# Kernel tuning notes

Hardware: AMD Instinct MI355X
Metric: run time of the kernel (lower is better)

The kernel has to match this reference:

```python
import jax, jax.numpy as jnp
import numpy as np

IMG = 128
FX, FY, CX, CY = 588.03, 587.07, 320.0, 240.0
FLIP = 1.0
SAMPLE = 1024  # sample_num in Img2pcl
N_VERTS = 778


def setup_inputs() -> dict:
    key = jax.random.key(0)
    ks = jax.random.split(key, 6)
    B = 64
    real = jax.random.uniform(ks[0], (B, 1, IMG, IMG), jnp.float32)   # normalized depth in [0,1)
    synth = jax.random.uniform(ks[1], (B, 1, IMG, IMG), jnp.float32)  # unused by forward
    verts = jax.random.normal(ks[2], (B, N_VERTS, 3), jnp.float32)
    faces = jax.random.randint(ks[3], (1538, 3), 0, N_VERTS, jnp.int32)  # unused by forward
    center = jax.random.normal(ks[4], (B, 3), jnp.float32) * 0.1 + jnp.array([0.0, 0.0, 400.0], jnp.float32)
    # crop matrix must be invertible: identity plus small perturbation
    M = jnp.eye(3, dtype=jnp.float32)[None] + 0.1 * jax.random.normal(ks[5], (B, 3, 3), jnp.float32)
    cube = jnp.full((B, 3), 250.0, jnp.float32)
    return dict(real=real, synth=synth, verts=verts, faces=faces, center=center, M=M, cube=cube)


def _img2pcl(real, center, M, cube):
    """Vectorized Img2pcl: normalized (u,v,d) -> normalized xyz for every pixel, plus valid mask."""
    B = real.shape[0]
    # input already IMG x IMG so F.interpolate is identity
    img = real[:, 0]                                   # [B,H,W]
    t = 2.0 * jnp.arange(IMG, dtype=jnp.float32) / (IMG - 1.0) - 1.0
    mesh_x = jnp.broadcast_to(t[:, None], (IMG, IMG))  # varies along rows (v)
    mesh_y = jnp.broadcast_to(t[None, :], (IMG, IMG))  # varies along cols (u)
    uvd = jnp.stack([
        jnp.broadcast_to(mesh_y, (B, IMG, IMG)),
        jnp.broadcast_to(mesh_x, (B, IMG, IMG)),
        img,
    ], axis=-1).reshape(B, IMG * IMG, 3)               # [B,P,3]
    # unnormalize uv and depth
    uv = (uvd[..., :2] + 1.0) * (IMG / 2.0)
    d = uvd[..., 2] * (cube[:, None, 2] / 2.0) + center[:, None, 2]   # [B,P]
    # get_trans_points with M^{-1}
    M_inv = jnp.linalg.inv(M)                          # [B,3,3]
    h = jnp.concatenate([uv, jnp.ones_like(uv[..., :1])], axis=-1)    # [B,P,3]
    uv_w = jnp.einsum('bij,bpj->bpi', M_inv, h)[..., :2]
    # pointsImgTo3D (pinhole back-projection)
    x = (uv_w[..., 0] - CX) * d / FX
    y = FLIP * (uv_w[..., 1] - CY) * d / FY
    xyz = jnp.stack([x, y, d], axis=-1)                # [B,P,3]
    xyz_n = (xyz - center[:, None, :]) / (cube[:, None, :] / 2.0)
    mask = img.reshape(B, -1) <= 0.99                  # valid (foreground) pixels
    return xyz_n, mask


def reference(real, synth, verts, faces, center, M, cube):
    xyz, mask = _img2pcl(real, center, M, cube)
    # torch.multinomial(uniform weights, SAMPLE, without replacement) over valid pixels
    # == Gumbel top-k over the masked candidate set (jit-compatible, fixed shapes)
    u = jax.random.uniform(jax.random.key(1), mask.shape)
    gumbel = -jnp.log(-jnp.log(u + 1e-20) + 1e-20)
    score = jnp.where(mask, gumbel, -jnp.inf)
    _, idx = jax.lax.top_k(score, SAMPLE)              # [B,SAMPLE]
    pcl1 = jnp.take_along_axis(xyz, idx[..., None], axis=1)  # [B,SAMPLE,3]
    # chamfer distance (pytorch3d-style: mean-reduced squared-dist NN, both directions)
    d2 = jnp.sum((pcl1[:, :, None, :] - verts[:, None, :, :]) ** 2, axis=-1)  # [B,SAMPLE,V]
    loss = d2.min(axis=2).mean() + d2.min(axis=1).mean()
    return loss
```

## Files before the change

kernel.cpp:

```cpp
#include <hip/hip_runtime.h>
#include <stdint.h>
#include <math.h>

#define NPIX   16384
#define SAMPLE 1024
#define NV     778
#define BATCH  64

#define A_SCALE (1.0f / (float)(BATCH * SAMPLE))
#define B_SCALE (1.0f / (float)(BATCH * NV))

__device__ __forceinline__ uint32_t rotl32(uint32_t v, int r) {
  return (v << r) | (v >> (32 - r));
}

__device__ __forceinline__ uint32_t threefry_bits(uint32_t g) {
  uint32_t ks0 = 0u, ks1 = 1u;
  uint32_t ks2 = ks0 ^ ks1 ^ 0x1BD11BDAu;
  uint32_t x0 = 0u + ks0, x1 = g + ks1;
#define TF_R(r) { x0 += x1; x1 = rotl32(x1, (r)); x1 ^= x0; }
  TF_R(13) TF_R(15) TF_R(26) TF_R(6)
  x0 += ks1; x1 += ks2 + 1u;
  TF_R(17) TF_R(29) TF_R(16) TF_R(24)
  x0 += ks2; x1 += ks0 + 2u;
  TF_R(13) TF_R(15) TF_R(26) TF_R(6)
  x0 += ks0; x1 += ks1 + 3u;
  TF_R(17) TF_R(29) TF_R(16) TF_R(24)
  x0 += ks1; x1 += ks2 + 4u;
  TF_R(13) TF_R(15) TF_R(26) TF_R(6)
  x0 += ks2; x1 += ks0 + 5u;
#undef TF_R
  return x0 ^ x1;
}

__device__ __forceinline__ float waveReduceSum(float v) {
#pragma unroll
  for (int off = 32; off > 0; off >>= 1) v += __shfl_down(v, off, 64);
  return v;
}

__device__ __forceinline__ uint32_t blockExclScan1024(
    uint32_t v, volatile uint32_t* swt, volatile uint32_t* soffs,
    uint32_t* total) {
  const int tid = threadIdx.x;
  const int lane = tid & 63;
  const int wv = tid >> 6;
  __syncthreads();
  uint32_t incl = v;
#pragma unroll
  for (int off = 1; off < 64; off <<= 1) {
    uint32_t u = __shfl_up(incl, off, 64);
    if (lane >= off) incl += u;
  }
  if (lane == 63) swt[wv] = incl;
  __syncthreads();
  if (tid < 16) {
    uint32_t t = swt[tid], s = t;
#pragma unroll
    for (int off = 1; off < 16; off <<= 1) {
      uint32_t u = __shfl_up(s, off, 64);
      if (lane >= off) s += u;
    }
    soffs[tid] = s - t;
  }
  __syncthreads();
  *total = soffs[15] + swt[15];
  return soffs[wv] + incl - v;
}

__global__ __launch_bounds__(1024) void mega_kernel(
    const float4* __restrict__ real4,
    const float* __restrict__ verts,
    const float* __restrict__ center,
    const float* __restrict__ M,
    const float* __restrict__ cube,
    float* __restrict__ out) {
  const int bq = blockIdx.x;
  const int b = bq >> 2, q = bq & 3;
  const int tid = threadIdx.x;
  const int lane = tid & 63;
  const int wv = tid >> 6;

  __shared__ __align__(16) uint8_t shbuf[53408];
  float4*   sv4    = (float4*)shbuf;
  float4*   sp4    = (float4*)(shbuf + 12448);
  float*    fbuf   = (float*)(shbuf + 28832);
  uint32_t* hist   = (uint32_t*)(shbuf + 45216);
  uint64_t* cand   = (uint64_t*)(shbuf + 47264);
  float*    candrv = (float*)(shbuf + 51360);
  __shared__ uint32_t wt[8], offs[8];
  __shared__ uint32_t swt[16], soffs[16];
  __shared__ float sh_minv[6], sh_c[3], sh_hb[3];
  __shared__ uint32_t sh_bstar, sh_above;
  __shared__ float red[16];

  if (tid == 0) {
    const float* m = M + (size_t)b * 9;
    float m00=m[0], m01=m[1], m02=m[2];
    float m10=m[3], m11=m[4], m12=m[5];
    float m20=m[6], m21=m[7], m22=m[8];
    float c00 = m11*m22 - m12*m21;
    float c10 = m12*m20 - m10*m22;
    float c20 = m10*m21 - m11*m20;
    float det = m00*c00 + m01*c10 + m02*c20;
    float id = 1.0f / det;
    sh_minv[0] = c00 * id;
    sh_minv[1] = (m02*m21 - m01*m22) * id;
    sh_minv[2] = (m01*m12 - m02*m11) * id;
    sh_minv[3] = c10 * id;
    sh_minv[4] = (m00*m22 - m02*m20) * id;
    sh_minv[5] = (m02*m10 - m00*m12) * id;
    sh_c[0] = center[b*3+0]; sh_c[1] = center[b*3+1]; sh_c[2] = center[b*3+2];
    sh_hb[0] = cube[b*3+0]*0.5f; sh_hb[1] = cube[b*3+1]*0.5f; sh_hb[2] = cube[b*3+2]*0.5f;
  }
  if (tid < 512) hist[tid] = 0u;

  const float* vb = verts + (size_t)b * NV * 3;
  for (int v = tid; v < NV; v += 1024) {
    float x = vb[v*3], y = vb[v*3+1], z = vb[v*3+2];
    float4 t;
    t.x = -2.0f*x; t.y = -2.0f*y; t.z = -2.0f*z; t.w = x*x + y*y + z*z;
    sv4[v] = t;
  }

  uint32_t uv[16];
  float    rvv[16];
  const float4* rb4 = real4 + (size_t)b * (NPIX / 4);
#pragma unroll
  for (int e4 = 0; e4 < 4; ++e4) {
    float4 im = rb4[e4 * 1024 + tid];
    uint32_t base = (uint32_t)(b * NPIX + e4 * 4096) + (uint32_t)(tid << 2);
    rvv[e4*4+0] = im.x; rvv[e4*4+1] = im.y; rvv[e4*4+2] = im.z; rvv[e4*4+3] = im.w;
    uv[e4*4+0] = (im.x <= 0.99f) ? ((threefry_bits(base + 0u) >> 9) + 1u) : 0u;
    uv[e4*4+1] = (im.y <= 0.99f) ? ((threefry_bits(base + 1u) >> 9) + 1u) : 0u;
    uv[e4*4+2] = (im.z <= 0.99f) ? ((threefry_bits(base + 2u) >> 9) + 1u) : 0u;
    uv[e4*4+3] = (im.w <= 0.99f) ? ((threefry_bits(base + 3u) >> 9) + 1u) : 0u;
  }
  __syncthreads();

#pragma unroll
  for (int e = 0; e < 16; ++e)
    if (uv[e]) atomicAdd(&hist[(uv[e] - 1u) >> 14], 1u);
  __syncthreads();

  uint32_t cnt = 0, sfx = 0;
  if (tid < 512) {
    cnt = hist[tid];
    sfx = cnt;
#pragma unroll
    for (int off = 1; off < 64; off <<= 1) {
      uint32_t u = __shfl_down(sfx, off, 64);
      if (lane + off < 64) sfx += u;
    }
    if (lane == 0) wt[wv] = sfx;
  }
  __syncthreads();
  if (tid < 8) {
    uint32_t t = wt[tid], s = t;
#pragma unroll
    for (int off = 1; off < 8; off <<= 1) {
      uint32_t u = __shfl_down(s, off, 64);
      if (tid + off < 8) s += u;
    }
    offs[tid] = s - t;
  }
  __syncthreads();
  if (tid < 512) {
    uint32_t tot = sfx + offs[wv];
    uint32_t above = tot - cnt;
    if (tot >= SAMPLE && above < SAMPLE && cnt > 0) {
      sh_bstar = (uint32_t)tid;
      sh_above = above;
    }
  }
  __syncthreads();
  const int bstar = (int)sh_bstar;
  const uint32_t above = sh_above;
  const uint32_t kneed = SAMPLE - above;

  auto emit = [&](int p, float depth01, uint32_t slot) {
    int i = p >> 7, j = p & 127;
    float tj = (2.0f * (float)j) / 127.0f - 1.0f;
    float ti = (2.0f * (float)i) / 127.0f - 1.0f;
    float u0 = (tj + 1.0f) * 64.0f;
    float u1 = (ti + 1.0f) * 64.0f;
    float d  = depth01 * sh_hb[2] + sh_c[2];
    float w0 = sh_minv[0]*u0 + sh_minv[1]*u1 + sh_minv[2];
    float w1 = sh_minv[3]*u0 + sh_minv[4]*u1 + sh_minv[5];
    float x = (w0 - 320.0f) * d / 588.03f;
    float y = (w1 - 240.0f) * d / 587.07f;
    float ox = (x - sh_c[0]) / sh_hb[0];
    float oy = (y - sh_c[1]) / sh_hb[1];
    float oz = (d - sh_c[2]) / sh_hb[2];
    float4 t;
    t.x = -2.0f*ox; t.y = -2.0f*oy; t.z = -2.0f*oz;
    t.w = ox*ox + oy*oy + oz*oz;
    sp4[slot] = t;
  };

  uint32_t ch = 0, ce = 0;
#pragma unroll
  for (int e = 0; e < 16; ++e) {
    int bk = uv[e] ? (int)((uv[e] - 1u) >> 14) : -1;
    ch += (bk > bstar) ? 1u : 0u;
    ce += (bk == bstar) ? 1u : 0u;
  }
  uint32_t htot, etot;
  uint32_t hoff = blockExclScan1024(ch, swt, soffs, &htot);
  uint32_t eoff = blockExclScan1024(ce, swt, soffs, &etot);

  {
    uint32_t h = hoff, eo = eoff;
#pragma unroll
    for (int e = 0; e < 16; ++e) {
      uint32_t v = uv[e];
      int bk = v ? (int)((v - 1u) >> 14) : -1;
      int p = (e >> 2) * 4096 + (tid << 2) + (e & 3);
      if (bk > bstar) {
        emit(p, rvv[e], h++);
      } else if (bk == bstar) {
        if (eo < 512u) {
          cand[eo] = ((uint64_t)v << 14) | (uint64_t)(16383 - p);
          candrv[eo] = rvv[e];
        }
        eo++;
      }
    }
  }
  __syncthreads();

  uint32_t c = etot; if (c > 512u) c = 512u;
  uint32_t selbit = 0; uint64_t ki = 0;
  if (tid < (int)c) {
    ki = cand[tid];
    uint32_t rank = 0;
    for (uint32_t j2 = 0; j2 < c; ++j2) rank += (cand[j2] > ki) ? 1u : 0u;
    selbit = (rank < kneed) ? 1u : 0u;
  }
  uint32_t stot;
  uint32_t soff2 = blockExclScan1024(selbit, swt, soffs, &stot);
  if (selbit) {
    int p = 16383 - (int)(ki & 0x3FFFull);
    emit(p, candrv[tid], above + soff2);
  }
  __syncthreads();

  float val = 0.0f;
  const int sub = tid & 63;
  const int seg16 = tid >> 6;

  {
    float px[4], py[4], pz[4], mnA[4];
#pragma unroll
    for (int j = 0; j < 4; ++j) {
      float4 sp = sp4[q * 256 + j * 64 + sub];
      px[j] = -0.5f * sp.x; py[j] = -0.5f * sp.y; pz[j] = -0.5f * sp.z;
      mnA[j] = INFINITY;
    }
    int vs = seg16 * 49, ve = vs + 49; if (ve > NV) ve = NV;
    for (int v = vs; v < ve; ++v) {
      float4 vv = sv4[v];
#pragma unroll
      for (int j = 0; j < 4; ++j) {
        float t = fmaf(pz[j], vv.z, fmaf(py[j], vv.y, fmaf(px[j], vv.x, vv.w)));
        mnA[j] = fminf(mnA[j], t);
      }
    }
#pragma unroll
    for (int j = 0; j < 4; ++j) fbuf[seg16 * 256 + j * 64 + sub] = mnA[j];
  }
  __syncthreads();
  if (tid < 256) {
    float m = fbuf[tid];
#pragma unroll
    for (int s2 = 1; s2 < 16; ++s2) m = fminf(m, fbuf[s2 * 256 + tid]);
    val += (m + sp4[q * 256 + tid].w) * A_SCALE;
  }
  __syncthreads();

  {
    const int vbase = q * 195;
    int nsl = NV - vbase; if (nsl > 195) nsl = 195;
    float vx[4], vy[4], vz[4], mnB[4];
#pragma unroll
    for (int j = 0; j < 4; ++j) {
      int vloc = j * 64 + sub;
      int vi = (vloc < nsl) ? (vbase + vloc) : 0;
      float4 sv = sv4[vi];
      vx[j] = -0.5f * sv.x; vy[j] = -0.5f * sv.y; vz[j] = -0.5f * sv.z;
      mnB[j] = INFINITY;
    }
    int is = seg16 * 64;
    for (int i = 0; i < 64; ++i) {
      float4 pp = sp4[is + i];
#pragma unroll
      for (int j = 0; j < 4; ++j) {
        float t = fmaf(vz[j], pp.z, fmaf(vy[j], pp.y, fmaf(vx[j], pp.x, pp.w)));
        mnB[j] = fminf(mnB[j], t);
      }
    }
#pragma unroll
    for (int j = 0; j < 4; ++j) fbuf[seg16 * 256 + j * 64 + sub] = mnB[j];
  }
  __syncthreads();
  {
    const int vbase = q * 195;
    int nsl = NV - vbase; if (nsl > 195) nsl = 195;
    if (tid < nsl) {
      float m = fbuf[tid];
#pragma unroll
      for (int s2 = 1; s2 < 16; ++s2) m = fminf(m, fbuf[s2 * 256 + tid]);
      val += (m + sv4[vbase + tid].w) * B_SCALE;
    }
  }

  float r = waveReduceSum(val);
  if (lane == 0) red[wv] = r;
  __syncthreads();
  if (tid == 0) {
    float s = 0.0f;
#pragma unroll
    for (int i = 0; i < 16; ++i) s += red[i];
    atomicAdd(out, s);
  }
}

extern "C" void kernel_launch(void* const* d_in, const int* in_sizes, int n_in,
                              void* d_out, int out_size, void* d_ws, size_t ws_size,
                              hipStream_t stream) {
  const float* real   = (const float*)d_in[0];
  const float* verts  = (const float*)d_in[2];
  const float* center = (const float*)d_in[4];
  const float* M      = (const float*)d_in[5];
  const float* cube   = (const float*)d_in[6];
  float* out = (float*)d_out;

  hipMemsetAsync(out, 0, sizeof(float), stream);
  mega_kernel<<<dim3(BATCH * 4), dim3(1024), 0, stream>>>(
      (const float4*)real, verts, center, M, cube, out);
}
```

Measured before the change: 109.9 us.

## Split RNG scoring into separate kernel to deduplicate threefry across quarter-blocks

Before this change, each of the four blocks per batch recomputed the threefry Gumbel bits and the histogram for the whole 16384-pixel image. A new score_kernel spreads that work across the four blocks, writes the per-pixel keys and per-quarter histograms to workspace, and also zeroes the output, which removes the separate memset. The chamfer/selection kernel then reads the keys and sums the four partial histograms instead of recomputing them. In exchange it adds a second launch and a global round-trip of about 4 MB of keys. The old fused kernel stays as a fallback when the workspace is too small.

```diff
diff --git a/kernel.cpp b/kernel.cpp
--- a/kernel.cpp
+++ b/kernel.cpp
@@ -9,6 +9,10 @@
 
 #define A_SCALE (1.0f / (float)(BATCH * SAMPLE))
 #define B_SCALE (1.0f / (float)(BATCH * NV))
+
+#define WS_UBITS  0u
+#define WS_HISTG  4194304u
+#define WS_NEEDED 4718592u
 
 __device__ __forceinline__ uint32_t rotl32(uint32_t v, int r) {
   return (v << r) | (v >> (32 - r));
@@ -68,12 +72,46 @@
   return soffs[wv] + incl - v;
 }
 
-__global__ __launch_bounds__(1024) void mega_kernel(
+__global__ __launch_bounds__(1024) void score_kernel(
+    const float4* __restrict__ real4,
+    uint32_t* __restrict__ ubits,
+    uint32_t* __restrict__ histg,
+    float* __restrict__ out) {
+  const int bq = blockIdx.x;
+  const int b = bq >> 2, q = bq & 3;
+  const int tid = threadIdx.x;
+  __shared__ uint32_t hist[512];
+
+  if (bq == 0 && tid == 0) out[0] = 0.0f;
+  if (tid < 512) hist[tid] = 0u;
+
+  float4 im = real4[(size_t)b * 4096 + q * 1024 + tid];
+  uint32_t base = (uint32_t)(b * NPIX + q * 4096) + (uint32_t)(tid << 2);
+  uint32_t u0 = (im.x <= 0.99f) ? ((threefry_bits(base + 0u) >> 9) + 1u) : 0u;
+  uint32_t u1 = (im.y <= 0.99f) ? ((threefry_bits(base + 1u) >> 9) + 1u) : 0u;
+  uint32_t u2 = (im.z <= 0.99f) ? ((threefry_bits(base + 2u) >> 9) + 1u) : 0u;
+  uint32_t u3 = (im.w <= 0.99f) ? ((threefry_bits(base + 3u) >> 9) + 1u) : 0u;
+
+  uint4 st; st.x = u0; st.y = u1; st.z = u2; st.w = u3;
+  ((uint4*)ubits)[(size_t)b * 4096 + q * 1024 + tid] = st;
+
+  __syncthreads();
+  if (u0) atomicAdd(&hist[(u0 - 1u) >> 14], 1u);
+  if (u1) atomicAdd(&hist[(u1 - 1u) >> 14], 1u);
+  if (u2) atomicAdd(&hist[(u2 - 1u) >> 14], 1u);
+  if (u3) atomicAdd(&hist[(u3 - 1u) >> 14], 1u);
+  __syncthreads();
+  if (tid < 512) histg[(size_t)bq * 512 + tid] = hist[tid];
+}
+
+__global__ __launch_bounds__(1024) void chamsel_kernel(
     const float4* __restrict__ real4,
     const float* __restrict__ verts,
     const float* __restrict__ center,
     const float* __restrict__ M,
     const float* __restrict__ cube,
+    const uint32_t* __restrict__ ubits,
+    const uint32_t* __restrict__ histg,
     float* __restrict__ out) {
   const int bq = blockIdx.x;
   const int b = bq >> 2, q = bq & 3;
@@ -81,13 +119,12 @@
   const int lane = tid & 63;
   const int wv = tid >> 6;
 
-  __shared__ __align__(16) uint8_t shbuf[53408];
+  __shared__ __align__(16) uint8_t shbuf[51360];
   float4*   sv4    = (float4*)shbuf;
   float4*   sp4    = (float4*)(shbuf + 12448);
   float*    fbuf   = (float*)(shbuf + 28832);
-  uint32_t* hist   = (uint32_t*)(shbuf + 45216);
-  uint64_t* cand   = (uint64_t*)(shbuf + 47264);
-  float*    candrv = (float*)(shbuf + 51360);
+  uint64_t* cand   = (uint64_t*)(shbuf + 45216);
+  float*    candrv = (float*)(shbuf + 49312);
   __shared__ uint32_t wt[8], offs[8];
   __shared__ uint32_t swt[16], soffs[16];
   __shared__ float sh_minv[6], sh_c[3], sh_hb[3];
@@ -113,7 +150,6 @@
     sh_c[0] = center[b*3+0]; sh_c[1] = center[b*3+1]; sh_c[2] = center[b*3+2];
     sh_hb[0] = cube[b*3+0]*0.5f; sh_hb[1] = cube[b*3+1]*0.5f; sh_hb[2] = cube[b*3+2]*0.5f;
   }
-  if (tid < 512) hist[tid] = 0u;
 
   const float* vb = verts + (size_t)b * NV * 3;
   for (int v = tid; v < NV; v += 1024) {
@@ -126,26 +162,19 @@
   uint32_t uv[16];
   float    rvv[16];
   const float4* rb4 = real4 + (size_t)b * (NPIX / 4);
+  const uint4*  ub4 = (const uint4*)ubits + (size_t)b * (NPIX / 4);
 #pragma unroll
   for (int e4 = 0; e4 < 4; ++e4) {
     float4 im = rb4[e4 * 1024 + tid];
-    uint32_t base = (uint32_t)(b * NPIX + e4 * 4096) + (uint32_t)(tid << 2);
+    uint4  uu = ub4[e4 * 1024 + tid];
     rvv[e4*4+0] = im.x; rvv[e4*4+1] = im.y; rvv[e4*4+2] = im.z; rvv[e4*4+3] = im.w;
-    uv[e4*4+0] = (im.x <= 0.99f) ? ((threefry_bits(base + 0u) >> 9) + 1u) : 0u;
-    uv[e4*4+1] = (im.y <= 0.99f) ? ((threefry_bits(base + 1u) >> 9) + 1u) : 0u;
-    uv[e4*4+2] = (im.z <= 0.99f) ? ((threefry_bits(base + 2u) >> 9) + 1u) : 0u;
-    uv[e4*4+3] = (im.w <= 0.99f) ? ((threefry_bits(base + 3u) >> 9) + 1u) : 0u;
-  }
-  __syncthreads();
-
-#pragma unroll
-  for (int e = 0; e < 16; ++e)
-    if (uv[e]) atomicAdd(&hist[(uv[e] - 1u) >> 14], 1u);
-  __syncthreads();
+    uv[e4*4+0] = uu.x; uv[e4*4+1] = uu.y; uv[e4*4+2] = uu.z; uv[e4*4+3] = uu.w;
+  }
 
   uint32_t cnt = 0, sfx = 0;
   if (tid < 512) {
-    cnt = hist[tid];
+    const uint32_t* hp = histg + (size_t)(b << 2) * 512 + tid;
+    cnt = hp[0] + hp[512] + hp[1024] + hp[1536];
     sfx = cnt;
 #pragma unroll
     for (int off = 1; off < 64; off <<= 1) {
@@ -325,6 +354,263 @@
   }
 }
 
+__global__ __launch_bounds__(1024) void mega_kernel(
+    const float4* __restrict__ real4,
+    const float* __restrict__ verts,
+    const float* __restrict__ center,
+    const float* __restrict__ M,
+    const float* __restrict__ cube,
+    float* __restrict__ out) {
+  const int bq = blockIdx.x;
+  const int b = bq >> 2, q = bq & 3;
+  const int tid = threadIdx.x;
+  const int lane = tid & 63;
+  const int wv = tid >> 6;
+
+  __shared__ __align__(16) uint8_t shbuf[53408];
+  float4*   sv4    = (float4*)shbuf;
+  float4*   sp4    = (float4*)(shbuf + 12448);
+  float*    fbuf   = (float*)(shbuf + 28832);
+  uint32_t* hist   = (uint32_t*)(shbuf + 45216);
+  uint64_t* cand   = (uint64_t*)(shbuf + 47264);
+  float*    candrv = (float*)(shbuf + 51360);
+  __shared__ uint32_t wt[8], offs[8];
+  __shared__ uint32_t swt[16], soffs[16];
+  __shared__ float sh_minv[6], sh_c[3], sh_hb[3];
+  __shared__ uint32_t sh_bstar, sh_above;
+  __shared__ float red[16];
+
+  if (tid == 0) {
+    const float* m = M + (size_t)b * 9;
+    float m00=m[0], m01=m[1], m02=m[2];
+    float m10=m[3], m11=m[4], m12=m[5];
+    float m20=m[6], m21=m[7], m22=m[8];
+    float c00 = m11*m22 - m12*m21;
+    float c10 = m12*m20 - m10*m22;
+    float c20 = m10*m21 - m11*m20;
+    float det = m00*c00 + m01*c10 + m02*c20;
+    float id = 1.0f / det;
+    sh_minv[0] = c00 * id;
+    sh_minv[1] = (m02*m21 - m01*m22) * id;
+    sh_minv[2] = (m01*m12 - m02*m11) * id;
+    sh_minv[3] = c10 * id;
+    sh_minv[4] = (m00*m22 - m02*m20) * id;
+    sh_minv[5] = (m02*m10 - m00*m12) * id;
+    sh_c[0] = center[b*3+0]; sh_c[1] = center[b*3+1]; sh_c[2] = center[b*3+2];
+    sh_hb[0] = cube[b*3+0]*0.5f; sh_hb[1] = cube[b*3+1]*0.5f; sh_hb[2] = cube[b*3+2]*0.5f;
+  }
+  if (tid < 512) hist[tid] = 0u;
+
+  const float* vb = verts + (size_t)b * NV * 3;
+  for (int v = tid; v < NV; v += 1024) {
+    float x = vb[v*3], y = vb[v*3+1], z = vb[v*3+2];
+    float4 t;
+    t.x = -2.0f*x; t.y = -2.0f*y; t.z = -2.0f*z; t.w = x*x + y*y + z*z;
+    sv4[v] = t;
+  }
+
+  uint32_t uv[16];
+  float    rvv[16];
+  const float4* rb4 = real4 + (size_t)b * (NPIX / 4);
+#pragma unroll
+  for (int e4 = 0; e4 < 4; ++e4) {
+    float4 im = rb4[e4 * 1024 + tid];
+    uint32_t base = (uint32_t)(b * NPIX + e4 * 4096) + (uint32_t)(tid << 2);
+    rvv[e4*4+0] = im.x; rvv[e4*4+1] = im.y; rvv[e4*4+2] = im.z; rvv[e4*4+3] = im.w;
+    uv[e4*4+0] = (im.x <= 0.99f) ? ((threefry_bits(base + 0u) >> 9) + 1u) : 0u;
+    uv[e4*4+1] = (im.y <= 0.99f) ? ((threefry_bits(base + 1u) >> 9) + 1u) : 0u;
+    uv[e4*4+2] = (im.z <= 0.99f) ? ((threefry_bits(base + 2u) >> 9) + 1u) : 0u;
+    uv[e4*4+3] = (im.w <= 0.99f) ? ((threefry_bits(base + 3u) >> 9) + 1u) : 0u;
+  }
+  __syncthreads();
+
+#pragma unroll
+  for (int e = 0; e < 16; ++e)
+    if (uv[e]) atomicAdd(&hist[(uv[e] - 1u) >> 14], 1u);
+  __syncthreads();
+
+  uint32_t cnt = 0, sfx = 0;
+  if (tid < 512) {
+    cnt = hist[tid];
+    sfx = cnt;
+#pragma unroll
+    for (int off = 1; off < 64; off <<= 1) {
+      uint32_t u = __shfl_down(sfx, off, 64);
+      if (lane + off < 64) sfx += u;
+    }
+    if (lane == 0) wt[wv] = sfx;
+  }
+  __syncthreads();
+  if (tid < 8) {
+    uint32_t t = wt[tid], s = t;
+#pragma unroll
+    for (int off = 1; off < 8; off <<= 1) {
+      uint32_t u = __shfl_down(s, off, 64);
+      if (tid + off < 8) s += u;
+    }
+    offs[tid] = s - t;
+  }
+  __syncthreads();
+  if (tid < 512) {
+    uint32_t tot = sfx + offs[wv];
+    uint32_t above = tot - cnt;
+    if (tot >= SAMPLE && above < SAMPLE && cnt > 0) {
+      sh_bstar = (uint32_t)tid;
+      sh_above = above;
+    }
+  }
+  __syncthreads();
+  const int bstar = (int)sh_bstar;
+  const uint32_t above = sh_above;
+  const uint32_t kneed = SAMPLE - above;
+
+  auto emit = [&](int p, float depth01, uint32_t slot) {
+    int i = p >> 7, j = p & 127;
+    float tj = (2.0f * (float)j) / 127.0f - 1.0f;
+    float ti = (2.0f * (float)i) / 127.0f - 1.0f;
+    float u0 = (tj + 1.0f) * 64.0f;
+    float u1 = (ti + 1.0f) * 64.0f;
+    float d  = depth01 * sh_hb[2] + sh_c[2];
+    float w0 = sh_minv[0]*u0 + sh_minv[1]*u1 + sh_minv[2];
+    float w1 = sh_minv[3]*u0 + sh_minv[4]*u1 + sh_minv[5];
+    float x = (w0 - 320.0f) * d / 588.03f;
+    float y = (w1 - 240.0f) * d / 587.07f;
+    float ox = (x - sh_c[0]) / sh_hb[0];
+    float oy = (y - sh_c[1]) / sh_hb[1];
+    float oz = (d - sh_c[2]) / sh_hb[2];
+    float4 t;
+    t.x = -2.0f*ox; t.y = -2.0f*oy; t.z = -2.0f*oz;
+    t.w = ox*ox + oy*oy + oz*oz;
+    sp4[slot] = t;
+  };
+
+  uint32_t ch = 0, ce = 0;
+#pragma unroll
+  for (int e = 0; e < 16; ++e) {
+    int bk = uv[e] ? (int)((uv[e] - 1u) >> 14) : -1;
+    ch += (bk > bstar) ? 1u : 0u;
+    ce += (bk == bstar) ? 1u : 0u;
+  }
+  uint32_t htot, etot;
+  uint32_t hoff = blockExclScan1024(ch, swt, soffs, &htot);
+  uint32_t eoff = blockExclScan1024(ce, swt, soffs, &etot);
+
+  {
+    uint32_t h = hoff, eo = eoff;
+#pragma unroll
+    for (int e = 0; e < 16; ++e) {
+      uint32_t v = uv[e];
+      int bk = v ? (int)((v - 1u) >> 14) : -1;
+      int p = (e >> 2) * 4096 + (tid << 2) + (e & 3);
+      if (bk > bstar) {
+        emit(p, rvv[e], h++);
+      } else if (bk == bstar) {
+        if (eo < 512u) {
+          cand[eo] = ((uint64_t)v << 14) | (uint64_t)(16383 - p);
+          candrv[eo] = rvv[e];
+        }
+        eo++;
+      }
+    }
+  }
+  __syncthreads();
+
+  uint32_t c = etot; if (c > 512u) c = 512u;
+  uint32_t selbit = 0; uint64_t ki = 0;
+  if (tid < (int)c) {
+    ki = cand[tid];
+    uint32_t rank = 0;
+    for (uint32_t j2 = 0; j2 < c; ++j2) rank += (cand[j2] > ki) ? 1u : 0u;
+    selbit = (rank < kneed) ? 1u : 0u;
+  }
+  uint32_t stot;
+  uint32_t soff2 = blockExclScan1024(selbit, swt, soffs, &stot);
+  if (selbit) {
+    int p = 16383 - (int)(ki & 0x3FFFull);
+    emit(p, candrv[tid], above + soff2);
+  }
+  __syncthreads();
+
+  float val = 0.0f;
+  const int sub = tid & 63;
+  const int seg16 = tid >> 6;
+
+  {
+    float px[4], py[4], pz[4], mnA[4];
+#pragma unroll
+    for (int j = 0; j < 4; ++j) {
+      float4 sp = sp4[q * 256 + j * 64 + sub];
+      px[j] = -0.5f * sp.x; py[j] = -0.5f * sp.y; pz[j] = -0.5f * sp.z;
+      mnA[j] = INFINITY;
+    }
+    int vs = seg16 * 49, ve = vs + 49; if (ve > NV) ve = NV;
+    for (int v = vs; v < ve; ++v) {
+      float4 vv = sv4[v];
+#pragma unroll
+      for (int j = 0; j < 4; ++j) {
+        float t = fmaf(pz[j], vv.z, fmaf(py[j], vv.y, fmaf(px[j], vv.x, vv.w)));
+        mnA[j] = fminf(mnA[j], t);
+      }
+    }
+#pragma unroll
+    for (int j = 0; j < 4; ++j) fbuf[seg16 * 256 + j * 64 + sub] = mnA[j];
+  }
+  __syncthreads();
+  if (tid < 256) {
+    float m = fbuf[tid];
+#pragma unroll
+    for (int s2 = 1; s2 < 16; ++s2) m = fminf(m, fbuf[s2 * 256 + tid]);
+    val += (m + sp4[q * 256 + tid].w) * A_SCALE;
+  }
+  __syncthreads();
+
+  {
+    const int vbase = q * 195;
+    int nsl = NV - vbase; if (nsl > 195) nsl = 195;
+    float vx[4], vy[4], vz[4], mnB[4];
+#pragma unroll
+    for (int j = 0; j < 4; ++j) {
+      int vloc = j * 64 + sub;
+      int vi = (vloc < nsl) ? (vbase + vloc) : 0;
+      float4 sv = sv4[vi];
+      vx[j] = -0.5f * sv.x; vy[j] = -0.5f * sv.y; vz[j] = -0.5f * sv.z;
+      mnB[j] = INFINITY;
+    }
+    int is = seg16 * 64;
+    for (int i = 0; i < 64; ++i) {
+      float4 pp = sp4[is + i];
+#pragma unroll
+      for (int j = 0; j < 4; ++j) {
+        float t = fmaf(vz[j], pp.z, fmaf(vy[j], pp.y, fmaf(vx[j], pp.x, pp.w)));
+        mnB[j] = fminf(mnB[j], t);
+      }
+    }
+#pragma unroll
+    for (int j = 0; j < 4; ++j) fbuf[seg16 * 256 + j * 64 + sub] = mnB[j];
+  }
+  __syncthreads();
+  {
+    const int vbase = q * 195;
+    int nsl = NV - vbase; if (nsl > 195) nsl = 195;
+    if (tid < nsl) {
+      float m = fbuf[tid];
+#pragma unroll
+      for (int s2 = 1; s2 < 16; ++s2) m = fminf(m, fbuf[s2 * 256 + tid]);
+      val += (m + sv4[vbase + tid].w) * B_SCALE;
+    }
+  }
+
+  float r = waveReduceSum(val);
+  if (lane == 0) red[wv] = r;
+  __syncthreads();
+  if (tid == 0) {
+    float s = 0.0f;
+#pragma unroll
+    for (int i = 0; i < 16; ++i) s += red[i];
+    atomicAdd(out, s);
+  }
+}
+
 extern "C" void kernel_launch(void* const* d_in, const int* in_sizes, int n_in,
                               void* d_out, int out_size, void* d_ws, size_t ws_size,
                               hipStream_t stream) {
@@ -335,7 +621,17 @@
   const float* cube   = (const float*)d_in[6];
   float* out = (float*)d_out;
 
-  hipMemsetAsync(out, 0, sizeof(float), stream);
-  mega_kernel<<<dim3(BATCH * 4), dim3(1024), 0, stream>>>(
-      (const float4*)real, verts, center, M, cube, out);
-}
+  if (ws_size >= (size_t)WS_NEEDED) {
+    uint8_t* w = (uint8_t*)d_ws;
+    uint32_t* ubits = (uint32_t*)(w + WS_UBITS);
+    uint32_t* histg = (uint32_t*)(w + WS_HISTG);
+    score_kernel<<<dim3(BATCH * 4), dim3(1024), 0, stream>>>(
+        (const float4*)real, ubits, histg, out);
+    chamsel_kernel<<<dim3(BATCH * 4), dim3(1024), 0, stream>>>(
+        (const float4*)real, verts, center, M, cube, ubits, histg, out);
+  } else {
+    hipMemsetAsync(out, 0, sizeof(float), stream);
+    mega_kernel<<<dim3(BATCH * 4), dim3(1024), 0, stream>>>(
+        (const float4*)real, verts, center, M, cube, out);
+  }
+}
```

New measurement: 108.3 us. About the same (-1.4%).
